# Performance work log

Measured on AMD Instinct MI355X. Metric: run time of the kernel, lower is better.

## Reference

```python
import jax, jax.numpy as jnp
import numpy as np
import math

B, T, C = 4, 2048, 1024
NH, D = 16, 64  # n_head, head_dim; NH * D == C


def setup_inputs() -> dict:
    key = jax.random.key(0)
    ks = jax.random.split(key, 7)
    std = 0.02
    return {
        "x": jax.random.normal(ks[0], (B, T, C), dtype=jnp.float32),
        "W_attn": jax.random.normal(ks[1], (C, 3 * C), dtype=jnp.float32) * std,
        "b_attn": jax.random.normal(ks[2], (3 * C,), dtype=jnp.float32) * std,
        "bQ": jax.random.normal(ks[3], (NH, D), dtype=jnp.float32) * 0.1 + 0.5,
        "bK": jax.random.normal(ks[4], (NH, D), dtype=jnp.float32) * 0.1 + 0.3,
        "W_proj": jax.random.normal(ks[5], (C, C), dtype=jnp.float32) * std,
        "b_proj": jax.random.normal(ks[6], (C,), dtype=jnp.float32) * std,
    }


def reference(x, W_attn, b_attn, bQ, bK, W_proj, b_proj):
    Bx, Tx, Cx = x.shape
    qkv = x @ W_attn + b_attn                      # [B, T, 3C]
    q, k, v = jnp.split(qkv, 3, axis=2)
    # [B, T, C] -> [B, NH, T, D]
    q = q.reshape(Bx, Tx, NH, D).transpose(0, 2, 1, 3)
    k = k.reshape(Bx, Tx, NH, D).transpose(0, 2, 1, 3)
    v = v.reshape(Bx, Tx, NH, D).transpose(0, 2, 1, 3)
    # per-head disorder bias added to Q and K before the dot product
    q = q + bQ[None, :, None, :]
    k = k + bK[None, :, None, :]
    scores = jnp.einsum('bhqd,bhkd->bhqk', q, k) / math.sqrt(D)  # [B, NH, T, T]
    causal = jnp.tril(jnp.ones((Tx, Tx), dtype=bool))
    scores = jnp.where(causal[None, None], scores, jnp.float32(-jnp.inf))
    att = jax.nn.softmax(scores, axis=-1)
    y = jnp.einsum('bhqk,bhkd->bhqd', att, v)      # [B, NH, T, D]
    y = y.transpose(0, 2, 1, 3).reshape(Bx, Tx, Cx)
    return y @ W_proj + b_proj
```

## Files before the change

kernel.cpp:

```cpp
#include <hip/hip_runtime.h>

typedef unsigned short u16;
typedef unsigned int u32;
typedef unsigned long long u64;
typedef __bf16 bf16x8 __attribute__((ext_vector_type(8)));
typedef float f32x4 __attribute__((ext_vector_type(4)));

#define B_  4
#define T_  2048
#define C_  1024
#define NH_ 16
#define D_  64
#define M_  (B_*T_)
#define N_QKV (3*C_)

#define ATTN_BLOCKS 1024

#define BARRIER()  __asm__ __volatile__("s_barrier" ::: "memory")
#define WAIT_VM4() __asm__ __volatile__("s_waitcnt vmcnt(4)" ::: "memory")
#define WAIT_VM8() __asm__ __volatile__("s_waitcnt vmcnt(8)" ::: "memory")
#define WAIT_VM0() __asm__ __volatile__("s_waitcnt vmcnt(0)" ::: "memory")
#define LGKM0()    __asm__ __volatile__("s_waitcnt lgkmcnt(0)" ::: "memory")

__device__ __forceinline__ void async_copy16(void* lds, const void* gptr) {
  __builtin_amdgcn_global_load_lds(
      (const __attribute__((address_space(1))) u32*)gptr,
      (__attribute__((address_space(3))) u32*)(u32)(uintptr_t)lds,
      16, 0, 0);
}

__device__ __forceinline__ u16 f2bf(float f) {
  union { float f; unsigned u; } c; c.f = f;
  unsigned u = c.u;
  unsigned r = (u + 0x7fffu + ((u >> 16) & 1u)) >> 16;
  return (u16)r;
}

__global__ __launch_bounds__(256) void conv_bf16(const float* __restrict__ in,
                                                 u16* __restrict__ out, int n) {
  int i = (blockIdx.x * 256 + threadIdx.x) * 4;
  if (i < n) {
    float4 f = *reinterpret_cast<const float4*>(in + i);
    u16 o[4] = { f2bf(f.x), f2bf(f.y), f2bf(f.z), f2bf(f.w) };
    *reinterpret_cast<uint2*>(out + i) = *reinterpret_cast<uint2*>(o);
  }
}

__global__ __launch_bounds__(256) void transpose_bf16(const float* __restrict__ in,
                                                      u16* __restrict__ out,
                                                      int K, int N) {
  __shared__ float tile[32][33];
  int bi = blockIdx.y;
  int bj = blockIdx.x;
  int tx = threadIdx.x & 31;
  int ty = threadIdx.x >> 5;
#pragma unroll
  for (int i = 0; i < 4; ++i) {
    int row = ty + i * 8;
    tile[row][tx] = in[(bi * 32 + row) * N + bj * 32 + tx];
  }
  __syncthreads();
#pragma unroll
  for (int i = 0; i < 4; ++i) {
    int row = ty + i * 8;
    out[(bj * 32 + row) * K + bi * 32 + tx] = f2bf(tile[tx][row]);
  }
}

__global__ __launch_bounds__(256, 2) void gemm_qkv(const u16* __restrict__ A,
                                                   const u16* __restrict__ Bt,
                                                   const float* __restrict__ b_attn,
                                                   const float* __restrict__ bQ,
                                                   const float* __restrict__ bK,
                                                   u16* __restrict__ qo,
                                                   u16* __restrict__ ko,
                                                   u16* __restrict__ vo) {
  const int K = C_;
  int bid = blockIdx.x;
  int wg = (bid & 7) * 192 + (bid >> 3);
  int bm = wg / 24, bn = wg % 24;

  int tid = threadIdx.x;
  int wid = tid >> 6, lane = tid & 63;
  int lm = lane & 15, lq = lane >> 4;
  int wm = (wid >> 1) * 64, wn = (wid & 1) * 64;

  __shared__ u16 As[2][128 * 64];
  __shared__ u16 Bs[2][128 * 64];

  f32x4 acc[4][4];
#pragma unroll
  for (int i = 0; i < 4; ++i)
#pragma unroll
    for (int j = 0; j < 4; ++j) acc[i][j] = (f32x4){0.f, 0.f, 0.f, 0.f};

  const u16* Ab = A + (size_t)(bm * 128) * K;
  const u16* Bb = Bt + (size_t)(bn * 128) * K;
  int srow = lane >> 3;
  int sgc  = ((lane & 7) ^ srow) * 8;

  auto stage = [&](int bb, int t) {
#pragma unroll
    for (int i = 0; i < 4; ++i) {
      int c = i * 4 + wid;
      async_copy16(&As[bb][c * 512], Ab + (size_t)(c * 8 + srow) * K + t * 64 + sgc);
      async_copy16(&Bs[bb][c * 512], Bb + (size_t)(c * 8 + srow) * K + t * 64 + sgc);
    }
  };

  stage(0, 0);
  const int NT = K / 64;
  for (int t = 0; t < NT; ++t) {
    int bb = t & 1;
    int tn = (t + 1 < NT) ? t + 1 : t;
    stage(bb ^ 1, tn);
    WAIT_VM8();
    BARRIER();
    bf16x8 af[4][2], bf[4][2];
#pragma unroll
    for (int mt = 0; mt < 4; ++mt) {
      const u16* base = &As[bb][(wm + mt * 16 + lm) * 64];
#pragma unroll
      for (int kh = 0; kh < 2; ++kh)
        af[mt][kh] = *reinterpret_cast<const bf16x8*>(base + (((kh * 4 + lq) ^ (lm & 7)) * 8));
    }
#pragma unroll
    for (int nt = 0; nt < 4; ++nt) {
      const u16* base = &Bs[bb][(wn + nt * 16 + lm) * 64];
#pragma unroll
      for (int kh = 0; kh < 2; ++kh)
        bf[nt][kh] = *reinterpret_cast<const bf16x8*>(base + (((kh * 4 + lq) ^ (lm & 7)) * 8));
    }
#pragma unroll
    for (int mt = 0; mt < 4; ++mt)
#pragma unroll
      for (int nt = 0; nt < 4; ++nt)
#pragma unroll
        for (int kh = 0; kh < 2; ++kh)
          acc[mt][nt] = __builtin_amdgcn_mfma_f32_16x16x32_bf16(af[mt][kh], bf[nt][kh],
                                                                acc[mt][nt], 0, 0, 0);
    LGKM0();
    BARRIER();
  }
  WAIT_VM0();

  const float qscale = 0.18033688011112042f;
#pragma unroll
  for (int mt = 0; mt < 4; ++mt) {
#pragma unroll
    for (int nt = 0; nt < 4; ++nt) {
#pragma unroll
      for (int r = 0; r < 4; ++r) {
        int m = bm * 128 + wm + mt * 16 + lq * 4 + r;
        int n = bn * 128 + wn + nt * 16 + lm;
        float val = acc[mt][nt][r] + b_attn[n];
        int sel = n >> 10;
        int c = n & 1023;
        int h = c >> 6;
        int d = c & 63;
        int b = m >> 11;
        int t = m & 2047;
        if (sel == 0)      qo[(((size_t)(b * NH_ + h) * T_) + t) * D_ + d] = f2bf((val + bQ[c]) * qscale);
        else if (sel == 1) ko[(((size_t)(b * NH_ + h) * T_) + t) * D_ + d] = f2bf(val + bK[c]);
        else               vo[(((size_t)(b * NH_ + h) * D_) + d) * T_ + t] = f2bf(val);
      }
    }
  }
}

__global__ __launch_bounds__(256, 4) void attn_kernel(const u16* __restrict__ q,
                                                      const u16* __restrict__ k,
                                                      const u16* __restrict__ vt,
                                                      u16* __restrict__ y) {
  int tid = threadIdx.x;
  int w = tid >> 6, lane = tid & 63;
  int lm = lane & 15, lq = lane >> 4;

  __shared__ u16 Ks[2][64 * 64];
  __shared__ u16 Vs[2][64 * 64];

  int srow = lane >> 3;
  int sg   = (lane & 7) ^ srow;

  int idx = blockIdx.x;
  int c8 = idx & 255, jq = idx >> 8;
  int a = c8 & 7, gq = c8 >> 3;
  int qt, bh;
  if (jq == 0)      { qt = 15 - a; bh = gq; }
  else if (jq == 1) { qt = 8 + a;  bh = 32 + gq; }
  else if (jq == 2) { qt = 7 - a;  bh = gq; }
  else              { qt = a;      bh = 32 + gq; }

  int b = bh >> 4, h = bh & 15;
  const int klast = 2 * qt + 1;
  const int qrow0 = qt * 128 + w * 32;

  const u16* qb = q + ((size_t)bh * T_ + qrow0) * D_;
  const u16* kb = k + (size_t)bh * T_ * D_;
  const u16* vb = vt + (size_t)bh * D_ * T_;

  auto stage_K = [&](int buf, int kbi) {
    const u16* gb = kb + (size_t)(kbi * 64) * 64;
#pragma unroll
    for (int j = 0; j < 2; ++j) {
      int c = w * 2 + j;
      async_copy16(&Ks[buf][c * 512], gb + (c * 8 + srow) * 64 + sg * 8);
    }
  };
  auto stage_V = [&](int buf, int kbi) {
    const u16* gb = vb + kbi * 64;
#pragma unroll
    for (int j = 0; j < 2; ++j) {
      int c = w * 2 + j;
      async_copy16(&Vs[buf][c * 512], gb + (size_t)(c * 8 + srow) * T_ + sg * 8);
    }
  };

  bf16x8 bq[2][2];
#pragma unroll
  for (int qt2 = 0; qt2 < 2; ++qt2) {
    const u16* qp = qb + (qt2 * 16 + lm) * D_ + lq * 8;
    bq[qt2][0] = *reinterpret_cast<const bf16x8*>(qp);
    bq[qt2][1] = *reinterpret_cast<const bf16x8*>(qp + 32);
  }

  const __bf16 one_ = (__bf16)1.0f;
  const bf16x8 ones = (bf16x8){one_, one_, one_, one_, one_, one_, one_, one_};

  f32x4 o[4][2], o5[2];
#pragma unroll
  for (int dt = 0; dt < 4; ++dt)
#pragma unroll
    for (int qt2 = 0; qt2 < 2; ++qt2) o[dt][qt2] = (f32x4){0.f, 0.f, 0.f, 0.f};
  o5[0] = (f32x4){0.f, 0.f, 0.f, 0.f};
  o5[1] = (f32x4){0.f, 0.f, 0.f, 0.f};
  float mprev[2] = {-1e30f, -1e30f};

  stage_K(0, 0); stage_V(0, 0);
  stage_K(1, 1); stage_V(1, 1);

  for (int kbi = 0; kbi <= klast; ++kbi) {
    int buf = kbi & 1;
    WAIT_VM4();
    BARRIER();

    bf16x8 kf[4][2];
#pragma unroll
    for (int kt = 0; kt < 4; ++kt) {
      const u16* base = &Ks[buf][(kt * 16 + lm) * 64];
      kf[kt][0] = *reinterpret_cast<const bf16x8*>(base + ((lq ^ (lm & 7)) * 8));
      kf[kt][1] = *reinterpret_cast<const bf16x8*>(base + (((4 + lq) ^ (lm & 7)) * 8));
    }

    f32x4 s[4][2];
    __builtin_amdgcn_s_setprio(1);
#pragma unroll
    for (int kt = 0; kt < 4; ++kt)
#pragma unroll
      for (int qt2 = 0; qt2 < 2; ++qt2) {
        f32x4 z = (f32x4){0.f, 0.f, 0.f, 0.f};
        z = __builtin_amdgcn_mfma_f32_16x16x32_bf16(kf[kt][0], bq[qt2][0], z, 0, 0, 0);
        z = __builtin_amdgcn_mfma_f32_16x16x32_bf16(kf[kt][1], bq[qt2][1], z, 0, 0, 0);
        s[kt][qt2] = z;
      }
    __builtin_amdgcn_s_setprio(0);

    bool maskt = (kbi * 64 + 63 > qrow0);
    bf16x8 pb[2][2];
#pragma unroll
    for (int qt2 = 0; qt2 < 2; ++qt2) {
      int qg = qrow0 + qt2 * 16 + lm;
      if (maskt) {
#pragma unroll
        for (int kt = 0; kt < 4; ++kt)
#pragma unroll
          for (int r = 0; r < 4; ++r) {
            int key = kbi * 64 + kt * 16 + lq * 4 + r;
            if (key > qg) s[kt][qt2][r] = -1e30f;
          }
      }
      float mx[4];
#pragma unroll
      for (int kt = 0; kt < 4; ++kt)
        mx[kt] = fmaxf(fmaxf(s[kt][qt2][0], s[kt][qt2][1]),
                       fmaxf(s[kt][qt2][2], s[kt][qt2][3]));
      float mval = fmaxf(fmaxf(mx[0], mx[1]), fmaxf(mx[2], mx[3]));
      mval = fmaxf(mval, __shfl_xor(mval, 16));
      mval = fmaxf(mval, __shfl_xor(mval, 32));
      float mold = mprev[qt2];
      if (__ballot(mval > mold + 8.f)) {
        float mnew = fmaxf(mold, mval);
        float alpha = __builtin_exp2f(mold - mnew);
#pragma unroll
        for (int dt = 0; dt < 4; ++dt) o[dt][qt2] *= alpha;
        o5[qt2] *= alpha;
        mprev[qt2] = mnew;
      }
      float m = mprev[qt2];
      unsigned pw[8];
#pragma unroll
      for (int kt = 0; kt < 4; ++kt) {
        unsigned pu[4];
#pragma unroll
        for (int r = 0; r < 4; ++r) {
          float p = __builtin_exp2f(s[kt][qt2][r] - m);
          union { float f; unsigned u; } cc; cc.f = p;
          pu[r] = cc.u;
        }
        pw[kt * 2]     = __builtin_amdgcn_perm(pu[1], pu[0], 0x07060302u);
        pw[kt * 2 + 1] = __builtin_amdgcn_perm(pu[3], pu[2], 0x07060302u);
      }
      union { unsigned u[4]; bf16x8 v; } b0, b1;
#pragma unroll
      for (int t = 0; t < 4; ++t) { b0.u[t] = pw[t]; b1.u[t] = pw[4 + t]; }
      pb[qt2][0] = b0.v;
      pb[qt2][1] = b1.v;
    }

    {
      int r7 = lm & 7;
      int h4 = (lq & 1) * 4;
      int g0 = lq >> 1;
#pragma unroll
      for (int dt = 0; dt < 4; ++dt) {
        const u16* vbase = &Vs[buf][(dt * 16 + lm) * 64];
        union { u64 qd[2]; bf16x8 v; } t0, t1;
        t0.qd[0] = *reinterpret_cast<const u64*>(vbase + ((g0 ^ r7) * 8) + h4);
        t0.qd[1] = *reinterpret_cast<const u64*>(vbase + (((g0 + 2) ^ r7) * 8) + h4);
        t1.qd[0] = *reinterpret_cast<const u64*>(vbase + (((g0 + 4) ^ r7) * 8) + h4);
        t1.qd[1] = *reinterpret_cast<const u64*>(vbase + (((g0 + 6) ^ r7) * 8) + h4);
        __builtin_amdgcn_s_setprio(1);
#pragma unroll
        for (int qt2 = 0; qt2 < 2; ++qt2) {
          o[dt][qt2] = __builtin_amdgcn_mfma_f32_16x16x32_bf16(t0.v, pb[qt2][0], o[dt][qt2], 0, 0, 0);
          o[dt][qt2] = __builtin_amdgcn_mfma_f32_16x16x32_bf16(t1.v, pb[qt2][1], o[dt][qt2], 0, 0, 0);
        }
        __builtin_amdgcn_s_setprio(0);
      }
#pragma unroll
      for (int qt2 = 0; qt2 < 2; ++qt2) {
        o5[qt2] = __builtin_amdgcn_mfma_f32_16x16x32_bf16(ones, pb[qt2][0], o5[qt2], 0, 0, 0);
        o5[qt2] = __builtin_amdgcn_mfma_f32_16x16x32_bf16(ones, pb[qt2][1], o5[qt2], 0, 0, 0);
      }
    }

    BARRIER();
    int nk = (kbi + 2 <= klast) ? kbi + 2 : klast;
    stage_K(buf, nk); stage_V(buf, nk);
  }

  WAIT_VM0();

#pragma unroll
  for (int qt2 = 0; qt2 < 2; ++qt2) {
    float inv = 1.f / o5[qt2][0];
    int qg = qrow0 + qt2 * 16 + lm;
#pragma unroll
    for (int dt = 0; dt < 4; ++dt) {
      u16 wb[4];
#pragma unroll
      for (int r = 0; r < 4; ++r) wb[r] = f2bf(o[dt][qt2][r] * inv);
      int d = dt * 16 + lq * 4;
      *reinterpret_cast<uint2*>(&y[((size_t)(b * T_ + qg) * NH_ + h) * D_ + d]) =
          *reinterpret_cast<uint2*>(wb);
    }
  }
}

__global__ __launch_bounds__(256, 2) void gemm_proj(const u16* __restrict__ A,
                                                    const u16* __restrict__ Bt,
                                                    const float* __restrict__ b_proj,
                                                    float* __restrict__ out) {
  const int K = C_, N = C_;
  int bid = blockIdx.x;
  int wg = (bid & 7) * 64 + (bid >> 3);
  int bm = wg / 8, bn = wg % 8;

  int tid = threadIdx.x;
  int wid = tid >> 6, lane = tid & 63;
  int lm = lane & 15, lq = lane >> 4;
  int wm = (wid >> 1) * 64, wn = (wid & 1) * 64;

  __shared__ u16 As[2][128 * 64];
  __shared__ u16 Bs[2][128 * 64];

  f32x4 acc[4][4];
#pragma unroll
  for (int i = 0; i < 4; ++i)
#pragma unroll
    for (int j = 0; j < 4; ++j) acc[i][j] = (f32x4){0.f, 0.f, 0.f, 0.f};

  const u16* Ab = A + (size_t)(bm * 128) * K;
  const u16* Bb = Bt + (size_t)(bn * 128) * K;
  int srow = lane >> 3;
  int sgc  = ((lane & 7) ^ srow) * 8;

  auto stage = [&](int bb, int t) {
#pragma unroll
    for (int i = 0; i < 4; ++i) {
      int c = i * 4 + wid;
      async_copy16(&As[bb][c * 512], Ab + (size_t)(c * 8 + srow) * K + t * 64 + sgc);
      async_copy16(&Bs[bb][c * 512], Bb + (size_t)(c * 8 + srow) * K + t * 64 + sgc);
    }
  };

  stage(0, 0);
  const int NT = K / 64;
  for (int t = 0; t < NT; ++t) {
    int bb = t & 1;
    int tn = (t + 1 < NT) ? t + 1 : t;
    stage(bb ^ 1, tn);
    WAIT_VM8();
    BARRIER();
    bf16x8 af[4][2], bf[4][2];
#pragma unroll
    for (int mt = 0; mt < 4; ++mt) {
      const u16* base = &As[bb][(wm + mt * 16 + lm) * 64];
#pragma unroll
      for (int kh = 0; kh < 2; ++kh)
        af[mt][kh] = *reinterpret_cast<const bf16x8*>(base + (((kh * 4 + lq) ^ (lm & 7)) * 8));
    }
#pragma unroll
    for (int nt = 0; nt < 4; ++nt) {
      const u16* base = &Bs[bb][(wn + nt * 16 + lm) * 64];
#pragma unroll
      for (int kh = 0; kh < 2; ++kh)
        bf[nt][kh] = *reinterpret_cast<const bf16x8*>(base + (((kh * 4 + lq) ^ (lm & 7)) * 8));
    }
#pragma unroll
    for (int mt = 0; mt < 4; ++mt)
#pragma unroll
      for (int nt = 0; nt < 4; ++nt)
#pragma unroll
        for (int kh = 0; kh < 2; ++kh)
          acc[mt][nt] = __builtin_amdgcn_mfma_f32_16x16x32_bf16(af[mt][kh], bf[nt][kh],
                                                                acc[mt][nt], 0, 0, 0);
    LGKM0();
    BARRIER();
  }
  WAIT_VM0();

#pragma unroll
  for (int mt = 0; mt < 4; ++mt) {
#pragma unroll
    for (int nt = 0; nt < 4; ++nt) {
#pragma unroll
      for (int r = 0; r < 4; ++r) {
        int m = bm * 128 + wm + mt * 16 + lq * 4 + r;
        int n = bn * 128 + wn + nt * 16 + lm;
        out[(size_t)m * N + n] = acc[mt][nt][r] + b_proj[n];
      }
    }
  }
}

extern "C" void kernel_launch(void* const* d_in, const int* in_sizes, int n_in,
                              void* d_out, int out_size, void* d_ws, size_t ws_size,
                              hipStream_t stream) {
  const float* x      = (const float*)d_in[0];
  const float* W_attn = (const float*)d_in[1];
  const float* b_attn = (const float*)d_in[2];
  const float* bQ     = (const float*)d_in[3];
  const float* bK     = (const float*)d_in[4];
  const float* W_proj = (const float*)d_in[5];
  const float* b_proj = (const float*)d_in[6];
  float* out = (float*)d_out;

  char* ws = (char*)d_ws;
  u16* xb  = (u16*)(ws);
  u16* WaT = (u16*)(ws + 16777216);
  u16* WpT = (u16*)(ws + 23068672);
  u16* qw  = (u16*)(ws + 25165824);
  u16* kw  = (u16*)(ws + 41943040);
  u16* vw  = (u16*)(ws + 58720256);
  u16* yw  = (u16*)(ws + 75497472);

  conv_bf16<<<M_ * C_ / (4 * 256), 256, 0, stream>>>(x, xb, M_ * C_);
  {
    dim3 g(N_QKV / 32, C_ / 32);
    transpose_bf16<<<g, 256, 0, stream>>>(W_attn, WaT, C_, N_QKV);
  }
  {
    dim3 g(C_ / 32, C_ / 32);
    transpose_bf16<<<g, 256, 0, stream>>>(W_proj, WpT, C_, C_);
  }
  gemm_qkv<<<(M_ / 128) * (N_QKV / 128), 256, 0, stream>>>(xb, WaT, b_attn, bQ, bK, qw, kw, vw);
  attn_kernel<<<ATTN_BLOCKS, 256, 0, stream>>>(qw, kw, vw, yw);
  gemm_proj<<<(M_ / 128) * (C_ / 128), 256, 0, stream>>>(yw, WpT, b_proj, out);
}
```

Measured before the change: 325.7 us.

## Vectorize QKV epilogue stores, compute softmax row sums in ALU, drop setprio

For Q/K column blocks the QKV GEMM swaps its MFMA operands so each lane holds four consecutive head-dim values, which allows bias adds and packed 8-byte stores. V blocks also store four consecutive timesteps per lane. In attention, the softmax denominator is now accumulated with VALU adds and cross-lane shuffles instead of extra ones-vector MFMAs. The lazy rescale threshold is removed, so the running max is updated on every increase, and the s_setprio hints are dropped. The aim is fewer scattered 2-byte writes and fewer MFMA issues, at the cost of more shuffles and more frequent rescaling.

```diff
diff --git a/kernel.cpp b/kernel.cpp
--- a/kernel.cpp
+++ b/kernel.cpp
@@ -79,6 +79,7 @@
   int bid = blockIdx.x;
   int wg = (bid & 7) * 192 + (bid >> 3);
   int bm = wg / 24, bn = wg % 24;
+  const bool qk = (bn < 16);
 
   int tid = threadIdx.x;
   int wid = tid >> 6, lane = tid & 63;
@@ -131,38 +132,75 @@
       for (int kh = 0; kh < 2; ++kh)
         bf[nt][kh] = *reinterpret_cast<const bf16x8*>(base + (((kh * 4 + lq) ^ (lm & 7)) * 8));
     }
-#pragma unroll
-    for (int mt = 0; mt < 4; ++mt)
-#pragma unroll
-      for (int nt = 0; nt < 4; ++nt)
-#pragma unroll
-        for (int kh = 0; kh < 2; ++kh)
-          acc[mt][nt] = __builtin_amdgcn_mfma_f32_16x16x32_bf16(af[mt][kh], bf[nt][kh],
-                                                                acc[mt][nt], 0, 0, 0);
+    if (qk) {
+#pragma unroll
+      for (int mt = 0; mt < 4; ++mt)
+#pragma unroll
+        for (int nt = 0; nt < 4; ++nt)
+#pragma unroll
+          for (int kh = 0; kh < 2; ++kh)
+            acc[mt][nt] = __builtin_amdgcn_mfma_f32_16x16x32_bf16(bf[nt][kh], af[mt][kh],
+                                                                  acc[mt][nt], 0, 0, 0);
+    } else {
+#pragma unroll
+      for (int mt = 0; mt < 4; ++mt)
+#pragma unroll
+        for (int nt = 0; nt < 4; ++nt)
+#pragma unroll
+          for (int kh = 0; kh < 2; ++kh)
+            acc[mt][nt] = __builtin_amdgcn_mfma_f32_16x16x32_bf16(af[mt][kh], bf[nt][kh],
+                                                                  acc[mt][nt], 0, 0, 0);
+    }
     LGKM0();
     BARRIER();
   }
   WAIT_VM0();
 
   const float qscale = 0.18033688011112042f;
-#pragma unroll
-  for (int mt = 0; mt < 4; ++mt) {
-#pragma unroll
-    for (int nt = 0; nt < 4; ++nt) {
-#pragma unroll
-      for (int r = 0; r < 4; ++r) {
-        int m = bm * 128 + wm + mt * 16 + lq * 4 + r;
+  if (qk) {
+    const float* bvec = (bn < 8) ? bQ : bK;
+    u16* outp = (bn < 8) ? qo : ko;
+    float scale = (bn < 8) ? qscale : 1.0f;
+#pragma unroll
+    for (int mt = 0; mt < 4; ++mt) {
+#pragma unroll
+      for (int nt = 0; nt < 4; ++nt) {
+        int n0 = bn * 128 + wn + nt * 16 + lq * 4;
+        int m  = bm * 128 + wm + mt * 16 + lm;
+        int c0 = n0 & 1023;
+        int h = c0 >> 6;
+        int d0 = c0 & 63;
+        int b = m >> 11;
+        int tt = m & 2047;
+        float4 ba = *reinterpret_cast<const float4*>(&b_attn[n0]);
+        float4 bb = *reinterpret_cast<const float4*>(&bvec[c0]);
+        u16 wb[4];
+        wb[0] = f2bf((acc[mt][nt][0] + ba.x + bb.x) * scale);
+        wb[1] = f2bf((acc[mt][nt][1] + ba.y + bb.y) * scale);
+        wb[2] = f2bf((acc[mt][nt][2] + ba.z + bb.z) * scale);
+        wb[3] = f2bf((acc[mt][nt][3] + ba.w + bb.w) * scale);
+        *reinterpret_cast<uint2*>(&outp[((size_t)(b * NH_ + h) * T_ + tt) * D_ + d0]) =
+            *reinterpret_cast<uint2*>(wb);
+      }
+    }
+  } else {
+#pragma unroll
+    for (int mt = 0; mt < 4; ++mt) {
+#pragma unroll
+      for (int nt = 0; nt < 4; ++nt) {
+        int m0 = bm * 128 + wm + mt * 16 + lq * 4;
         int n = bn * 128 + wn + nt * 16 + lm;
-        float val = acc[mt][nt][r] + b_attn[n];
-        int sel = n >> 10;
         int c = n & 1023;
         int h = c >> 6;
         int d = c & 63;
-        int b = m >> 11;
-        int t = m & 2047;
-        if (sel == 0)      qo[(((size_t)(b * NH_ + h) * T_) + t) * D_ + d] = f2bf((val + bQ[c]) * qscale);
-        else if (sel == 1) ko[(((size_t)(b * NH_ + h) * T_) + t) * D_ + d] = f2bf(val + bK[c]);
-        else               vo[(((size_t)(b * NH_ + h) * D_) + d) * T_ + t] = f2bf(val);
+        int b = m0 >> 11;
+        int t0 = m0 & 2047;
+        float bias = b_attn[n];
+        u16 wb[4];
+#pragma unroll
+        for (int r = 0; r < 4; ++r) wb[r] = f2bf(acc[mt][nt][r] + bias);
+        *reinterpret_cast<uint2*>(&vo[((size_t)(b * NH_ + h) * D_ + d) * T_ + t0]) =
+            *reinterpret_cast<uint2*>(wb);
       }
     }
   }
@@ -224,17 +262,12 @@
     bq[qt2][1] = *reinterpret_cast<const bf16x8*>(qp + 32);
   }
 
-  const __bf16 one_ = (__bf16)1.0f;
-  const bf16x8 ones = (bf16x8){one_, one_, one_, one_, one_, one_, one_, one_};
-
-  f32x4 o[4][2], o5[2];
+  f32x4 o[4][2];
 #pragma unroll
   for (int dt = 0; dt < 4; ++dt)
 #pragma unroll
     for (int qt2 = 0; qt2 < 2; ++qt2) o[dt][qt2] = (f32x4){0.f, 0.f, 0.f, 0.f};
-  o5[0] = (f32x4){0.f, 0.f, 0.f, 0.f};
-  o5[1] = (f32x4){0.f, 0.f, 0.f, 0.f};
-  float mprev[2] = {-1e30f, -1e30f};
+  float mprev[2] = {-1e30f, -1e30f}, lsum[2] = {0.f, 0.f};
 
   stage_K(0, 0); stage_V(0, 0);
   stage_K(1, 1); stage_V(1, 1);
@@ -253,7 +286,6 @@
     }
 
     f32x4 s[4][2];
-    __builtin_amdgcn_s_setprio(1);
 #pragma unroll
     for (int kt = 0; kt < 4; ++kt)
 #pragma unroll
@@ -263,7 +295,6 @@
         z = __builtin_amdgcn_mfma_f32_16x16x32_bf16(kf[kt][1], bq[qt2][1], z, 0, 0, 0);
         s[kt][qt2] = z;
       }
-    __builtin_amdgcn_s_setprio(0);
 
     bool maskt = (kbi * 64 + 63 > qrow0);
     bf16x8 pb[2][2];
@@ -288,28 +319,33 @@
       mval = fmaxf(mval, __shfl_xor(mval, 16));
       mval = fmaxf(mval, __shfl_xor(mval, 32));
       float mold = mprev[qt2];
-      if (__ballot(mval > mold + 8.f)) {
-        float mnew = fmaxf(mold, mval);
+      float mnew = fmaxf(mold, mval);
+      unsigned long long upd = __ballot(mval > mold);
+      if (upd) {
         float alpha = __builtin_exp2f(mold - mnew);
+        lsum[qt2] *= alpha;
 #pragma unroll
         for (int dt = 0; dt < 4; ++dt) o[dt][qt2] *= alpha;
-        o5[qt2] *= alpha;
         mprev[qt2] = mnew;
       }
-      float m = mprev[qt2];
+      float rs = 0.f;
       unsigned pw[8];
 #pragma unroll
       for (int kt = 0; kt < 4; ++kt) {
         unsigned pu[4];
 #pragma unroll
         for (int r = 0; r < 4; ++r) {
-          float p = __builtin_exp2f(s[kt][qt2][r] - m);
+          float p = __builtin_exp2f(s[kt][qt2][r] - mnew);
+          rs += p;
           union { float f; unsigned u; } cc; cc.f = p;
           pu[r] = cc.u;
         }
         pw[kt * 2]     = __builtin_amdgcn_perm(pu[1], pu[0], 0x07060302u);
         pw[kt * 2 + 1] = __builtin_amdgcn_perm(pu[3], pu[2], 0x07060302u);
       }
+      rs += __shfl_xor(rs, 16);
+      rs += __shfl_xor(rs, 32);
+      lsum[qt2] += rs;
       union { unsigned u[4]; bf16x8 v; } b0, b1;
 #pragma unroll
       for (int t = 0; t < 4; ++t) { b0.u[t] = pw[t]; b1.u[t] = pw[4 + t]; }
@@ -329,18 +365,11 @@
         t0.qd[1] = *reinterpret_cast<const u64*>(vbase + (((g0 + 2) ^ r7) * 8) + h4);
         t1.qd[0] = *reinterpret_cast<const u64*>(vbase + (((g0 + 4) ^ r7) * 8) + h4);
         t1.qd[1] = *reinterpret_cast<const u64*>(vbase + (((g0 + 6) ^ r7) * 8) + h4);
-        __builtin_amdgcn_s_setprio(1);
 #pragma unroll
         for (int qt2 = 0; qt2 < 2; ++qt2) {
           o[dt][qt2] = __builtin_amdgcn_mfma_f32_16x16x32_bf16(t0.v, pb[qt2][0], o[dt][qt2], 0, 0, 0);
           o[dt][qt2] = __builtin_amdgcn_mfma_f32_16x16x32_bf16(t1.v, pb[qt2][1], o[dt][qt2], 0, 0, 0);
         }
-        __builtin_amdgcn_s_setprio(0);
-      }
-#pragma unroll
-      for (int qt2 = 0; qt2 < 2; ++qt2) {
-        o5[qt2] = __builtin_amdgcn_mfma_f32_16x16x32_bf16(ones, pb[qt2][0], o5[qt2], 0, 0, 0);
-        o5[qt2] = __builtin_amdgcn_mfma_f32_16x16x32_bf16(ones, pb[qt2][1], o5[qt2], 0, 0, 0);
       }
     }
 
@@ -353,7 +382,7 @@
 
 #pragma unroll
   for (int qt2 = 0; qt2 < 2; ++qt2) {
-    float inv = 1.f / o5[qt2][0];
+    float inv = 1.f / lsum[qt2];
     int qg = qrow0 + qt2 * 16 + lm;
 #pragma unroll
     for (int dt = 0; dt < 4; ++dt) {
```

Measured after the change: 285.9 us. -12.2%, faster.
